# Kernel optimization log

Measured on AMD Instinct MI355X. Metric: run time of the kernel, lower is better.

The kernel has to match this reference:

```python
import jax, jax.numpy as jnp
import numpy as np

B, S, H, I, E, K = 2, 2048, 1024, 2048, 8, 2


def setup_inputs() -> dict:
    key = jax.random.key(0)
    k1, k2, k3, k4, k5 = jax.random.split(key, 5)
    scale_h = 1.0 / np.sqrt(H)
    scale_i = 1.0 / np.sqrt(I)
    return {
        "x": jax.random.normal(k1, (B, S, H), dtype=jnp.float32),
        "Wg": jax.random.normal(k2, (H, E), dtype=jnp.float32) * scale_h,
        "W11": jax.random.normal(k3, (E, H, I), dtype=jnp.float32) * scale_h,
        "W12": jax.random.normal(k4, (E, H, I), dtype=jnp.float32) * scale_h,
        "W2": jax.random.normal(k5, (E, I, H), dtype=jnp.float32) * scale_i,
    }


def reference(x, Wg, W11, W12, W2):
    # Router: softmax over experts, then top-k with renormalization (+1e-8 as in torch ref)
    gate_scores = jax.nn.softmax(x @ Wg, axis=-1)          # [B,S,E]
    topk_scores, topk_idx = jax.lax.top_k(gate_scores, K)   # [B,S,K]
    topk_scores = topk_scores / (topk_scores.sum(-1, keepdims=True) + 1e-8)

    # Dense per-expert SwiGLU on all tokens (matches reference's masked-dense math)
    gate = jnp.einsum('bsh,ehi->bsei', x, W11)              # [B,S,E,I]
    value = jnp.einsum('bsh,ehi->bsei', x, W12)
    fused = (gate * jax.nn.sigmoid(gate)) * value           # SiLU(gate) * value
    expert_out = jnp.einsum('bsei,eih->bseh', fused, W2)    # [B,S,E,H]

    # Gather the top-k experts' outputs per token and combine with routing weights
    gathered = jnp.take_along_axis(expert_out, topk_idx[..., None], axis=2)  # [B,S,K,H]
    out = jnp.sum(topk_scores[..., None] * gathered, axis=2)                 # [B,S,H]
    return out
```

## Files before the change

### kernel.cpp

```cpp
#include <hip/hip_runtime.h>
#include <hip/hip_bf16.h>
#include <stdint.h>

#define B_ 2
#define S_ 2048
#define H_ 1024
#define I_ 2048
#define E_ 8
#define TOK (B_*S_)
#define PAIRS (TOK*2)
#define MAXBLK 80

typedef __bf16 bf16_t;
typedef __bf16 bf16x4 __attribute__((ext_vector_type(4)));
typedef __bf16 bf16x8 __attribute__((ext_vector_type(8)));
typedef float  f32x4  __attribute__((ext_vector_type(4)));

__device__ __forceinline__ void gl_lds16(const bf16_t* g, bf16_t* l) {
    __builtin_amdgcn_global_load_lds(
        (const __attribute__((address_space(1))) unsigned int*)g,
        (__attribute__((address_space(3))) unsigned int*)l, 16, 0, 0);
}

__global__ void router_kernel(const float* __restrict__ x, const float* __restrict__ Wg,
                              int* __restrict__ top2e, float* __restrict__ top2w,
                              int* __restrict__ counts) {
    int wave = threadIdx.x >> 6;
    int lane = threadIdx.x & 63;
    int t = blockIdx.x * 4 + wave;
    if (t >= TOK) return;
    float acc[E_];
#pragma unroll
    for (int e = 0; e < E_; e++) acc[e] = 0.f;
    const float* xrow = x + (size_t)t * H_;
    for (int j = 0; j < H_ / 64; j++) {
        int h = j * 64 + lane;
        float xv = xrow[h];
        const float4* wg = (const float4*)(Wg + (size_t)h * E_);
        float4 w0 = wg[0], w1 = wg[1];
        acc[0] += xv * w0.x; acc[1] += xv * w0.y; acc[2] += xv * w0.z; acc[3] += xv * w0.w;
        acc[4] += xv * w1.x; acc[5] += xv * w1.y; acc[6] += xv * w1.z; acc[7] += xv * w1.w;
    }
#pragma unroll
    for (int e = 0; e < E_; e++) {
#pragma unroll
        for (int m = 32; m >= 1; m >>= 1) acc[e] += __shfl_xor(acc[e], m, 64);
    }
    if (lane == 0) {
        float mx = acc[0];
        for (int e = 1; e < E_; e++) mx = fmaxf(mx, acc[e]);
        float p[E_]; float z = 0.f;
        for (int e = 0; e < E_; e++) { p[e] = __expf(acc[e] - mx); z += p[e]; }
        for (int e = 0; e < E_; e++) p[e] /= z;
        int i1 = 0; float p1 = p[0];
        for (int e = 1; e < E_; e++) if (p[e] > p1) { p1 = p[e]; i1 = e; }
        int i2 = -1; float p2 = -1.f;
        for (int e = 0; e < E_; e++) if (e != i1 && p[e] > p2) { p2 = p[e]; i2 = e; }
        float s = p1 + p2 + 1e-8f;
        top2e[t * 2]     = i1; top2e[t * 2 + 1] = i2;
        top2w[t * 2]     = p1 / s; top2w[t * 2 + 1] = p2 / s;
        atomicAdd(&counts[i1], 1);
        atomicAdd(&counts[i2], 1);
    }
}

__global__ void scan_kernel(const int* __restrict__ counts, int* __restrict__ offsets,
                            int* __restrict__ cursor, int* __restrict__ blk_e,
                            int* __restrict__ blk_m0, int* __restrict__ nblk) {
    if (threadIdx.x == 0 && blockIdx.x == 0) {
        int run = 0, b = 0;
        for (int e = 0; e < E_; e++) {
            offsets[e] = run; cursor[e] = run;
            int c = counts[e];
            for (int m0 = 0; m0 < c; m0 += 128) { blk_e[b] = e; blk_m0[b] = m0; b++; }
            run += c;
        }
        nblk[0] = b;
    }
}

__global__ void fill_kernel(const int* __restrict__ top2e, const float* __restrict__ top2w,
                            int* __restrict__ cursor, int* __restrict__ pair_tok,
                            float* __restrict__ pair_w) {
    int t = blockIdx.x * blockDim.x + threadIdx.x;
    if (t >= TOK) return;
#pragma unroll
    for (int k = 0; k < 2; k++) {
        int e = top2e[t * 2 + k];
        int pos = atomicAdd(&cursor[e], 1);
        pair_tok[pos] = t;
        pair_w[pos]   = top2w[t * 2 + k];
    }
}

__global__ void castx_kernel(const float* __restrict__ x, bf16_t* __restrict__ xb) {
    size_t i = ((size_t)blockIdx.x * blockDim.x + threadIdx.x) * 4;
    float4 v = *(const float4*)(x + i);
    bf16x4 o = { (bf16_t)v.x, (bf16_t)v.y, (bf16_t)v.z, (bf16_t)v.w };
    *(bf16x4*)(xb + i) = o;
}

__global__ __launch_bounds__(256) void transpose_cast_kernel(
    const float* __restrict__ src, bf16_t* __restrict__ dst, int R, int C) {
    __shared__ float tile[64][65];
    int e = blockIdx.z;
    const float* s = src + (size_t)e * R * C;
    bf16_t* d = dst + (size_t)e * R * C;
    int c0 = blockIdx.x * 64, r0 = blockIdx.y * 64;
    int t = threadIdx.x;
    int lr = t >> 4, lc = (t & 15) * 4;
#pragma unroll
    for (int j = 0; j < 4; j++) {
        int r = r0 + lr + j * 16;
        float4 v = *(const float4*)(s + (size_t)r * C + c0 + lc);
        tile[lr + j * 16][lc + 0] = v.x;
        tile[lr + j * 16][lc + 1] = v.y;
        tile[lr + j * 16][lc + 2] = v.z;
        tile[lr + j * 16][lc + 3] = v.w;
    }
    __syncthreads();
    int oc = t >> 2, os = (t & 3) * 8;
#pragma unroll
    for (int j = 0; j < 2; j++) {
        int base = os + j * 32;
        bf16x8 v;
#pragma unroll
        for (int k = 0; k < 8; k++) v[k] = (bf16_t)tile[base + k][oc];
        *(bf16x8*)(d + (size_t)(c0 + oc) * R + r0 + base) = v;
    }
}

__global__ __launch_bounds__(256) void gemm1_kernel(
    const bf16_t* __restrict__ xb,
    const bf16_t* __restrict__ W11t,
    const bf16_t* __restrict__ W12t,
    const int* __restrict__ counts, const int* __restrict__ offsets,
    const int* __restrict__ blk_e, const int* __restrict__ blk_m0,
    const int* __restrict__ nblk,
    const int* __restrict__ pair_tok,
    bf16_t* __restrict__ fused)
{
    int by = blockIdx.y;
    if (by >= nblk[0]) return;
    int e = blk_e[by];
    int m0 = blk_m0[by];
    int cnt = counts[e];
    int off = offsets[e];
    int n0 = blockIdx.x * 64;

    __shared__ __align__(16) bf16_t la[128 * 64];
    __shared__ __align__(16) bf16_t lb[128 * 64];

    int tid = threadIdx.x;
    int w = tid >> 6, lane = tid & 63;
    int lrow = lane >> 3, lcol = lane & 7;
    int scol = lcol ^ lrow;

    const bf16_t* aptr[4];
    const bf16_t* bptr[4];
#pragma unroll
    for (int it = 0; it < 4; it++) {
        int r = it * 32 + w * 8 + lrow;
        int grow = m0 + r;
        int tok = pair_tok[off + (grow < cnt ? grow : 0)];
        aptr[it] = xb + (size_t)tok * H_ + scol * 8;
        const bf16_t* base = (r < 64)
            ? (W11t + ((size_t)e * I_ + n0 + r) * H_)
            : (W12t + ((size_t)e * I_ + n0 + (r - 64)) * H_);
        bptr[it] = base + scol * 8;
    }

    f32x4 acc[2][8];
#pragma unroll
    for (int a = 0; a < 2; a++)
#pragma unroll
        for (int b = 0; b < 8; b++) acc[a][b] = (f32x4){0.f, 0.f, 0.f, 0.f};

    for (int k0 = 0; k0 < H_; k0 += 64) {
#pragma unroll
        for (int it = 0; it < 4; it++) {
            gl_lds16(aptr[it] + k0, &la[(it * 32 + w * 8) * 64]);
            gl_lds16(bptr[it] + k0, &lb[(it * 32 + w * 8) * 64]);
        }
        __syncthreads();
        int q8 = (lane >> 4) * 8;
        int c16 = lane & 15;
        int rx = c16 & 7;
#pragma unroll
        for (int kk = 0; kk < 64; kk += 32) {
            int slot = ((kk + q8) >> 3) ^ rx;
            bf16x8 af[2], bfr[8];
#pragma unroll
            for (int ms = 0; ms < 2; ms++)
                af[ms] = *(const bf16x8*)&la[(w * 32 + ms * 16 + c16) * 64 + slot * 8];
#pragma unroll
            for (int ns = 0; ns < 8; ns++)
                bfr[ns] = *(const bf16x8*)&lb[(ns * 16 + c16) * 64 + slot * 8];
#pragma unroll
            for (int ms = 0; ms < 2; ms++)
#pragma unroll
                for (int ns = 0; ns < 8; ns++)
                    acc[ms][ns] = __builtin_amdgcn_mfma_f32_16x16x32_bf16(
                        af[ms], bfr[ns], acc[ms][ns], 0, 0, 0);
        }
        __syncthreads();
    }

    int col = lane & 15;
#pragma unroll
    for (int ms = 0; ms < 2; ms++) {
#pragma unroll
        for (int ns = 0; ns < 4; ns++) {
            f32x4 g = acc[ms][ns], v = acc[ms][ns + 4];
#pragma unroll
            for (int r = 0; r < 4; r++) {
                int mrow = w * 32 + ms * 16 + (lane >> 4) * 4 + r;
                int grow = m0 + mrow;
                if (grow < cnt) {
                    float gg = g[r];
                    float f = gg * v[r] / (1.f + __expf(-gg));
                    int i = n0 + ns * 16 + col;
                    fused[(size_t)(off + grow) * I_ + i] = (bf16_t)f;
                }
            }
        }
    }
}

__global__ __launch_bounds__(256) void gemm2_kernel(
    const bf16_t* __restrict__ fused,
    const bf16_t* __restrict__ W2t,
    const int* __restrict__ counts, const int* __restrict__ offsets,
    const int* __restrict__ blk_e, const int* __restrict__ blk_m0,
    const int* __restrict__ nblk,
    const int* __restrict__ pair_tok, const float* __restrict__ pair_w,
    float* __restrict__ out)
{
    int by = blockIdx.y;
    if (by >= nblk[0]) return;
    int e = blk_e[by];
    int m0 = blk_m0[by];
    int cnt = counts[e];
    int off = offsets[e];
    int n0 = blockIdx.x * 128;

    __shared__ __align__(16) bf16_t la[128 * 64];
    __shared__ __align__(16) bf16_t lb[128 * 64];

    int tid = threadIdx.x;
    int w = tid >> 6, lane = tid & 63;
    int lrow = lane >> 3, lcol = lane & 7;
    int scol = lcol ^ lrow;

    const bf16_t* aptr[4];
    const bf16_t* bptr[4];
#pragma unroll
    for (int it = 0; it < 4; it++) {
        int r = it * 32 + w * 8 + lrow;
        int grow = m0 + r;
        if (grow >= cnt) grow = cnt - 1;
        aptr[it] = fused + (size_t)(off + grow) * I_ + scol * 8;
        bptr[it] = W2t + ((size_t)e * H_ + n0 + r) * I_ + scol * 8;
    }

    f32x4 acc[2][8];
#pragma unroll
    for (int a = 0; a < 2; a++)
#pragma unroll
        for (int b = 0; b < 8; b++) acc[a][b] = (f32x4){0.f, 0.f, 0.f, 0.f};

    for (int k0 = 0; k0 < I_; k0 += 64) {
#pragma unroll
        for (int it = 0; it < 4; it++) {
            gl_lds16(aptr[it] + k0, &la[(it * 32 + w * 8) * 64]);
            gl_lds16(bptr[it] + k0, &lb[(it * 32 + w * 8) * 64]);
        }
        __syncthreads();
        int q8 = (lane >> 4) * 8;
        int c16 = lane & 15;
        int rx = c16 & 7;
#pragma unroll
        for (int kk = 0; kk < 64; kk += 32) {
            int slot = ((kk + q8) >> 3) ^ rx;
            bf16x8 af[2], bfr[8];
#pragma unroll
            for (int ms = 0; ms < 2; ms++)
                af[ms] = *(const bf16x8*)&la[(w * 32 + ms * 16 + c16) * 64 + slot * 8];
#pragma unroll
            for (int ns = 0; ns < 8; ns++)
                bfr[ns] = *(const bf16x8*)&lb[(ns * 16 + c16) * 64 + slot * 8];
#pragma unroll
            for (int ms = 0; ms < 2; ms++)
#pragma unroll
                for (int ns = 0; ns < 8; ns++)
                    acc[ms][ns] = __builtin_amdgcn_mfma_f32_16x16x32_bf16(
                        af[ms], bfr[ns], acc[ms][ns], 0, 0, 0);
        }
        __syncthreads();
    }

    int col = lane & 15;
#pragma unroll
    for (int ms = 0; ms < 2; ms++) {
#pragma unroll
        for (int r = 0; r < 4; r++) {
            int mrow = w * 32 + ms * 16 + (lane >> 4) * 4 + r;
            int grow = m0 + mrow;
            if (grow < cnt) {
                int slot = off + grow;
                int tok = pair_tok[slot];
                float wt = pair_w[slot];
#pragma unroll
                for (int ns = 0; ns < 8; ns++) {
                    atomicAdd(&out[(size_t)tok * H_ + n0 + ns * 16 + col], wt * acc[ms][ns][r]);
                }
            }
        }
    }
}

extern "C" void kernel_launch(void* const* d_in, const int* in_sizes, int n_in,
                              void* d_out, int out_size, void* d_ws, size_t ws_size,
                              hipStream_t stream) {
    const float* x   = (const float*)d_in[0];
    const float* Wg  = (const float*)d_in[1];
    const float* W11 = (const float*)d_in[2];
    const float* W12 = (const float*)d_in[3];
    const float* W2  = (const float*)d_in[4];
    float* out = (float*)d_out;

    char* ws = (char*)d_ws;
    size_t o = 0;
    auto alloc = [&](size_t bytes) { size_t r = o; o = (o + bytes + 255) & ~(size_t)255; return r; };
    int*    counts   = (int*)(ws + alloc(E_ * 4));
    int*    offsets  = (int*)(ws + alloc(E_ * 4));
    int*    cursor   = (int*)(ws + alloc(E_ * 4));
    int*    blk_e    = (int*)(ws + alloc(MAXBLK * 4));
    int*    blk_m0   = (int*)(ws + alloc(MAXBLK * 4));
    int*    nblk     = (int*)(ws + alloc(4));
    int*    top2e    = (int*)(ws + alloc(TOK * 2 * 4));
    float*  top2w    = (float*)(ws + alloc(TOK * 2 * 4));
    int*    pair_tok = (int*)(ws + alloc(PAIRS * 4));
    float*  pair_w   = (float*)(ws + alloc(PAIRS * 4));
    bf16_t* xb       = (bf16_t*)(ws + alloc((size_t)TOK * H_ * 2));
    bf16_t* W11t     = (bf16_t*)(ws + alloc((size_t)E_ * I_ * H_ * 2));
    bf16_t* W12t     = (bf16_t*)(ws + alloc((size_t)E_ * I_ * H_ * 2));
    bf16_t* W2t      = (bf16_t*)(ws + alloc((size_t)E_ * I_ * H_ * 2));
    bf16_t* fusedbuf = (bf16_t*)(ws + alloc((size_t)PAIRS * I_ * 2));

    hipMemsetAsync(counts, 0, E_ * 4, stream);
    hipMemsetAsync(d_out, 0, (size_t)out_size * 4, stream);

    router_kernel<<<TOK / 4, 256, 0, stream>>>(x, Wg, top2e, top2w, counts);
    scan_kernel<<<1, 64, 0, stream>>>(counts, offsets, cursor, blk_e, blk_m0, nblk);
    fill_kernel<<<TOK / 256, 256, 0, stream>>>(top2e, top2w, cursor, pair_tok, pair_w);

    castx_kernel<<<(TOK * H_ / 4) / 256, 256, 0, stream>>>(x, xb);
    transpose_cast_kernel<<<dim3(I_ / 64, H_ / 64, E_), 256, 0, stream>>>(W11, W11t, H_, I_);
    transpose_cast_kernel<<<dim3(I_ / 64, H_ / 64, E_), 256, 0, stream>>>(W12, W12t, H_, I_);
    transpose_cast_kernel<<<dim3(H_ / 64, I_ / 64, E_), 256, 0, stream>>>(W2, W2t, I_, H_);

    gemm1_kernel<<<dim3(I_ / 64, MAXBLK), 256, 0, stream>>>(
        xb, W11t, W12t, counts, offsets, blk_e, blk_m0, nblk, pair_tok, fusedbuf);
    gemm2_kernel<<<dim3(H_ / 128, MAXBLK), 256, 0, stream>>>(
        fusedbuf, W2t, counts, offsets, blk_e, blk_m0, nblk, pair_tok, pair_w, out);
}
```

Baseline: 597.7 us.

## Switch grouped GEMMs to 32x32x16 MFMA with 2x2 wave tiling, widen gemm1 tile

```diff
diff --git a/kernel.cpp b/kernel.cpp
--- a/kernel.cpp
+++ b/kernel.cpp
@@ -15,6 +15,7 @@
 typedef __bf16 bf16x4 __attribute__((ext_vector_type(4)));
 typedef __bf16 bf16x8 __attribute__((ext_vector_type(8)));
 typedef float  f32x4  __attribute__((ext_vector_type(4)));
+typedef float  f32x16 __attribute__((ext_vector_type(16)));
 
 __device__ __forceinline__ void gl_lds16(const bf16_t* g, bf16_t* l) {
     __builtin_amdgcn_global_load_lds(
@@ -130,7 +131,7 @@
     }
 }
 
-__global__ __launch_bounds__(256) void gemm1_kernel(
+__global__ __launch_bounds__(256, 2) void gemm1_kernel(
     const bf16_t* __restrict__ xb,
     const bf16_t* __restrict__ W11t,
     const bf16_t* __restrict__ W12t,
@@ -146,80 +147,96 @@
     int m0 = blk_m0[by];
     int cnt = counts[e];
     int off = offsets[e];
-    int n0 = blockIdx.x * 64;
+    int n0 = blockIdx.x * 128;
 
     __shared__ __align__(16) bf16_t la[128 * 64];
-    __shared__ __align__(16) bf16_t lb[128 * 64];
+    __shared__ __align__(16) bf16_t lb[256 * 64];
 
     int tid = threadIdx.x;
     int w = tid >> 6, lane = tid & 63;
+    int wm = w >> 1, wn = w & 1;
     int lrow = lane >> 3, lcol = lane & 7;
     int scol = lcol ^ lrow;
 
-    const bf16_t* aptr[4];
-    const bf16_t* bptr[4];
+    const bf16_t* aptr[2];
+    const bf16_t* bptr[8];
+#pragma unroll
+    for (int it = 0; it < 2; it++) {
+        ;
+    }
+    const bf16_t* aptr4[4];
 #pragma unroll
     for (int it = 0; it < 4; it++) {
         int r = it * 32 + w * 8 + lrow;
         int grow = m0 + r;
         int tok = pair_tok[off + (grow < cnt ? grow : 0)];
-        aptr[it] = xb + (size_t)tok * H_ + scol * 8;
-        const bf16_t* base = (r < 64)
+        aptr4[it] = xb + (size_t)tok * H_ + scol * 8;
+    }
+#pragma unroll
+    for (int it = 0; it < 8; it++) {
+        int r = it * 32 + w * 8 + lrow;
+        const bf16_t* base = (r < 128)
             ? (W11t + ((size_t)e * I_ + n0 + r) * H_)
-            : (W12t + ((size_t)e * I_ + n0 + (r - 64)) * H_);
+            : (W12t + ((size_t)e * I_ + n0 + (r - 128)) * H_);
         bptr[it] = base + scol * 8;
     }
 
-    f32x4 acc[2][8];
+    f32x16 acc[2][4];
 #pragma unroll
     for (int a = 0; a < 2; a++)
 #pragma unroll
-        for (int b = 0; b < 8; b++) acc[a][b] = (f32x4){0.f, 0.f, 0.f, 0.f};
+        for (int b = 0; b < 4; b++) acc[a][b] = (f32x16)(0.f);
+
+    int r32 = lane & 31;
+    int khalf = lane >> 5;
+    int rx = r32 & 7;
 
     for (int k0 = 0; k0 < H_; k0 += 64) {
 #pragma unroll
-        for (int it = 0; it < 4; it++) {
-            gl_lds16(aptr[it] + k0, &la[(it * 32 + w * 8) * 64]);
+        for (int it = 0; it < 4; it++)
+            gl_lds16(aptr4[it] + k0, &la[(it * 32 + w * 8) * 64]);
+#pragma unroll
+        for (int it = 0; it < 8; it++)
             gl_lds16(bptr[it] + k0, &lb[(it * 32 + w * 8) * 64]);
-        }
         __syncthreads();
-        int q8 = (lane >> 4) * 8;
-        int c16 = lane & 15;
-        int rx = c16 & 7;
-#pragma unroll
-        for (int kk = 0; kk < 64; kk += 32) {
-            int slot = ((kk + q8) >> 3) ^ rx;
-            bf16x8 af[2], bfr[8];
+#pragma unroll
+        for (int t16 = 0; t16 < 4; t16++) {
+            int seg = t16 * 2 + khalf;
+            bf16x8 af[2], bfr[4];
+#pragma unroll
+            for (int ms = 0; ms < 2; ms++) {
+                int row = wm * 64 + ms * 32 + r32;
+                af[ms] = *(const bf16x8*)&la[row * 64 + (seg ^ rx) * 8];
+            }
+#pragma unroll
+            for (int ns = 0; ns < 2; ns++) {
+                int browg = wn * 64 + ns * 32 + r32;
+                bfr[ns]     = *(const bf16x8*)&lb[browg * 64 + (seg ^ rx) * 8];
+                bfr[ns + 2] = *(const bf16x8*)&lb[(browg + 128) * 64 + (seg ^ rx) * 8];
+            }
 #pragma unroll
             for (int ms = 0; ms < 2; ms++)
-                af[ms] = *(const bf16x8*)&la[(w * 32 + ms * 16 + c16) * 64 + slot * 8];
-#pragma unroll
-            for (int ns = 0; ns < 8; ns++)
-                bfr[ns] = *(const bf16x8*)&lb[(ns * 16 + c16) * 64 + slot * 8];
-#pragma unroll
-            for (int ms = 0; ms < 2; ms++)
-#pragma unroll
-                for (int ns = 0; ns < 8; ns++)
-                    acc[ms][ns] = __builtin_amdgcn_mfma_f32_16x16x32_bf16(
+#pragma unroll
+                for (int ns = 0; ns < 4; ns++)
+                    acc[ms][ns] = __builtin_amdgcn_mfma_f32_32x32x16_bf16(
                         af[ms], bfr[ns], acc[ms][ns], 0, 0, 0);
         }
         __syncthreads();
     }
 
-    int col = lane & 15;
 #pragma unroll
     for (int ms = 0; ms < 2; ms++) {
 #pragma unroll
-        for (int ns = 0; ns < 4; ns++) {
-            f32x4 g = acc[ms][ns], v = acc[ms][ns + 4];
-#pragma unroll
-            for (int r = 0; r < 4; r++) {
-                int mrow = w * 32 + ms * 16 + (lane >> 4) * 4 + r;
-                int grow = m0 + mrow;
+        for (int ns = 0; ns < 2; ns++) {
+            int i = n0 + wn * 64 + ns * 32 + r32;
+#pragma unroll
+            for (int reg = 0; reg < 16; reg++) {
+                int rrow = (reg & 3) + 8 * (reg >> 2) + 4 * khalf;
+                int grow = m0 + wm * 64 + ms * 32 + rrow;
                 if (grow < cnt) {
-                    float gg = g[r];
-                    float f = gg * v[r] / (1.f + __expf(-gg));
-                    int i = n0 + ns * 16 + col;
+                    float g = acc[ms][ns][reg];
+                    float v = acc[ms][ns + 2][reg];
+                    float f = g * v / (1.f + __expf(-g));
                     fused[(size_t)(off + grow) * I_ + i] = (bf16_t)f;
                 }
             }
@@ -227,7 +244,7 @@
     }
 }
 
-__global__ __launch_bounds__(256) void gemm2_kernel(
+__global__ __launch_bounds__(256, 3) void gemm2_kernel(
     const bf16_t* __restrict__ fused,
     const bf16_t* __restrict__ W2t,
     const int* __restrict__ counts, const int* __restrict__ offsets,
@@ -249,6 +266,7 @@
 
     int tid = threadIdx.x;
     int w = tid >> 6, lane = tid & 63;
+    int wm = w >> 1, wn = w & 1;
     int lrow = lane >> 3, lcol = lane & 7;
     int scol = lcol ^ lrow;
 
@@ -263,11 +281,15 @@
         bptr[it] = W2t + ((size_t)e * H_ + n0 + r) * I_ + scol * 8;
     }
 
-    f32x4 acc[2][8];
+    f32x16 acc[2][2];
 #pragma unroll
     for (int a = 0; a < 2; a++)
 #pragma unroll
-        for (int b = 0; b < 8; b++) acc[a][b] = (f32x4){0.f, 0.f, 0.f, 0.f};
+        for (int b = 0; b < 2; b++) acc[a][b] = (f32x16)(0.f);
+
+    int r32 = lane & 31;
+    int khalf = lane >> 5;
+    int rx = r32 & 7;
 
     for (int k0 = 0; k0 < I_; k0 += 64) {
 #pragma unroll
@@ -276,43 +298,44 @@
             gl_lds16(bptr[it] + k0, &lb[(it * 32 + w * 8) * 64]);
         }
         __syncthreads();
-        int q8 = (lane >> 4) * 8;
-        int c16 = lane & 15;
-        int rx = c16 & 7;
-#pragma unroll
-        for (int kk = 0; kk < 64; kk += 32) {
-            int slot = ((kk + q8) >> 3) ^ rx;
-            bf16x8 af[2], bfr[8];
+#pragma unroll
+        for (int t16 = 0; t16 < 4; t16++) {
+            int seg = t16 * 2 + khalf;
+            bf16x8 af[2], bfr[2];
+#pragma unroll
+            for (int ms = 0; ms < 2; ms++) {
+                int row = wm * 64 + ms * 32 + r32;
+                af[ms] = *(const bf16x8*)&la[row * 64 + (seg ^ rx) * 8];
+            }
+#pragma unroll
+            for (int ns = 0; ns < 2; ns++) {
+                int brow = wn * 64 + ns * 32 + r32;
+                bfr[ns] = *(const bf16x8*)&lb[brow * 64 + (seg ^ rx) * 8];
+            }
 #pragma unroll
             for (int ms = 0; ms < 2; ms++)
-                af[ms] = *(const bf16x8*)&la[(w * 32 + ms * 16 + c16) * 64 + slot * 8];
-#pragma unroll
-            for (int ns = 0; ns < 8; ns++)
-                bfr[ns] = *(const bf16x8*)&lb[(ns * 16 + c16) * 64 + slot * 8];
-#pragma unroll
-            for (int ms = 0; ms < 2; ms++)
-#pragma unroll
-                for (int ns = 0; ns < 8; ns++)
-                    acc[ms][ns] = __builtin_amdgcn_mfma_f32_16x16x32_bf16(
+#pragma unroll
+                for (int ns = 0; ns < 2; ns++)
+                    acc[ms][ns] = __builtin_amdgcn_mfma_f32_32x32x16_bf16(
                         af[ms], bfr[ns], acc[ms][ns], 0, 0, 0);
         }
         __syncthreads();
     }
 
-    int col = lane & 15;
 #pragma unroll
     for (int ms = 0; ms < 2; ms++) {
 #pragma unroll
-        for (int r = 0; r < 4; r++) {
-            int mrow = w * 32 + ms * 16 + (lane >> 4) * 4 + r;
-            int grow = m0 + mrow;
+        for (int reg = 0; reg < 16; reg++) {
+            int rrow = (reg & 3) + 8 * (reg >> 2) + 4 * khalf;
+            int grow = m0 + wm * 64 + ms * 32 + rrow;
             if (grow < cnt) {
                 int slot = off + grow;
                 int tok = pair_tok[slot];
                 float wt = pair_w[slot];
 #pragma unroll
-                for (int ns = 0; ns < 8; ns++) {
-                    atomicAdd(&out[(size_t)tok * H_ + n0 + ns * 16 + col], wt * acc[ms][ns][r]);
+                for (int ns = 0; ns < 2; ns++) {
+                    int h = n0 + wn * 64 + ns * 32 + r32;
+                    atomicAdd(&out[(size_t)tok * H_ + h], wt * acc[ms][ns][reg]);
                 }
             }
         }
@@ -360,7 +383,7 @@
     transpose_cast_kernel<<<dim3(I_ / 64, H_ / 64, E_), 256, 0, stream>>>(W12, W12t, H_, I_);
     transpose_cast_kernel<<<dim3(H_ / 64, I_ / 64, E_), 256, 0, stream>>>(W2, W2t, I_, H_);
 
-    gemm1_kernel<<<dim3(I_ / 64, MAXBLK), 256, 0, stream>>>(
+    gemm1_kernel<<<dim3(I_ / 128, MAXBLK), 256, 0, stream>>>(
         xb, W11t, W12t, counts, offsets, blk_e, blk_m0, nblk, pair_tok, fusedbuf);
     gemm2_kernel<<<dim3(H_ / 128, MAXBLK), 256, 0, stream>>>(
         fusedbuf, W2t, counts, offsets, blk_e, blk_m0, nblk, pair_tok, pair_w, out);
```

Measured after the change: 541.2 us. -9.5%, faster.
